# Optimization experiments

Measured on AMD Instinct MI355X. Metric: run time of the kernel, lower is better.

## Reference

```python
import jax, jax.numpy as jnp
import numpy as np

B, S, C, H, D = 2, 2048, 1024, 16, 64  # hidden C must equal H*D (value is a reshape of key_states)


def setup_inputs() -> dict:
    key = jax.random.key(0)
    ks = jax.random.split(key, 7)
    query_states = jax.random.normal(ks[0], (B, S, C), dtype=jnp.float32)
    key_states = jax.random.normal(ks[1], (B, S, C), dtype=jnp.float32)
    attention_mask = jax.random.randint(ks[2], (B, 1, 1, S), 0, 2).astype(jnp.int32)
    Wq = jax.random.normal(ks[3], (C, H, D), dtype=jnp.float32) * 0.02
    bq = jnp.zeros((H, D), dtype=jnp.float32)
    Wk = jax.random.normal(ks[4], (C, H, D), dtype=jnp.float32) * 0.02
    bk = jnp.zeros((H, D), dtype=jnp.float32)
    return {
        "query_states": query_states,
        "key_states": key_states,
        "attention_mask": attention_mask,
        "Wq": Wq,
        "bq": bq,
        "Wk": Wk,
        "bk": bk,
    }


def reference(query_states, key_states, attention_mask, Wq, bq, Wk, bk):
    # EinsumDense 'abc,cde->abde' with bias on 'de'
    q = jnp.einsum("bsc,chd->bshd", query_states, Wq) + bq  # [B,S,H,D]
    k = jnp.einsum("bsc,chd->bshd", key_states, Wk) + bk    # [B,S,H,D]
    # value is just key_states reshaped into head layout (no projection!)
    v = key_states.reshape(k.shape)                          # [B,S,H,D]
    # scale query by 1/sqrt(dk)
    q = q * jax.lax.rsqrt(jnp.asarray(D, q.dtype))
    # 'aecd,abcd->acbe': a=batch, c=head, b=query pos, e=key pos
    scores = jnp.einsum("bkhd,bqhd->bhqk", k, q)             # [B,H,Sq,Sk]
    mask = (1.0 - attention_mask.astype(scores.dtype)) * -10000.0
    scores = scores + mask
    probs = jax.nn.softmax(scores, axis=-1)
    # dropout is identity at training=False (default)
    # 'acbe,aecd->abcd': weighted sum of values over key positions
    out = jnp.einsum("bhqk,bkhd->bqhd", probs, v)            # [B,S,H,D]
    return out
```

## Files before the change

### kernel.cpp

```cpp
#include <hip/hip_runtime.h>

#define BSZ 2
#define SEQ 2048
#define CH  1024
#define NH  16
#define HD  64
#define LOG2E 1.4426950408889634f

typedef short  bf16x8 __attribute__((ext_vector_type(8)));
typedef short  bf16x4 __attribute__((ext_vector_type(4)));
typedef float  f32x4  __attribute__((ext_vector_type(4)));

__device__ __forceinline__ short f2bf(float f) {
    union { float f; unsigned u; } v; v.f = f;
    unsigned r = v.u + 0x7FFFu + ((v.u >> 16) & 1u);
    return (short)(r >> 16);
}
__device__ __forceinline__ short f2bf_fast(float f) {
    union { float f; unsigned u; } v; v.f = f;
    return (short)((v.u + 0x8000u) >> 16);
}

__global__ __launch_bounds__(256) void cast_bf16(
    const float* __restrict__ a, const float* __restrict__ b,
    short* __restrict__ da, short* __restrict__ db)
{
    const float* s = blockIdx.y ? b : a;
    short*       d = blockIdx.y ? db : da;
    long i = ((long)blockIdx.x * 256 + threadIdx.x) * 8;
    float4 v0 = *(const float4*)&s[i];
    float4 v1 = *(const float4*)&s[i + 4];
    bf16x8 o;
    o[0] = f2bf(v0.x); o[1] = f2bf(v0.y); o[2] = f2bf(v0.z); o[3] = f2bf(v0.w);
    o[4] = f2bf(v1.x); o[5] = f2bf(v1.y); o[6] = f2bf(v1.z); o[7] = f2bf(v1.w);
    *(bf16x8*)&d[i] = o;
}

__global__ __launch_bounds__(256) void transpose_cast(
    const float* __restrict__ src, short* __restrict__ dst,
    long sb0, long sb1, long db0, long db1, int srs, int drs)
{
    __shared__ float tile[64][65];
    const int z = blockIdx.z;
    const float* s = src + (long)(z >> 4) * sb0 + (long)(z & 15) * sb1;
    short*       d = dst + (long)(z >> 4) * db0 + (long)(z & 15) * db1;
    const int r0 = blockIdx.y * 64, c0 = blockIdx.x * 64;
    const int tid = threadIdx.x;
    const int r  = tid >> 2;
    const int c4 = (tid & 3) << 4;

    #pragma unroll
    for (int i = 0; i < 16; i += 4) {
        float4 v = *(const float4*)&s[(long)(r0 + r) * srs + c0 + c4 + i];
        tile[r][c4 + i + 0] = v.x;
        tile[r][c4 + i + 1] = v.y;
        tile[r][c4 + i + 2] = v.z;
        tile[r][c4 + i + 3] = v.w;
    }
    __syncthreads();
    bf16x8 o0, o1;
    #pragma unroll
    for (int i = 0; i < 8; i++) o0[i] = f2bf(tile[c4 + i][r]);
    #pragma unroll
    for (int i = 0; i < 8; i++) o1[i] = f2bf(tile[c4 + 8 + i][r]);
    *(bf16x8*)&d[(long)(c0 + r) * drs + r0 + c4 + 0] = o0;
    *(bf16x8*)&d[(long)(c0 + r) * drs + r0 + c4 + 8] = o1;
}

__global__ __launch_bounds__(256) void mask_prep(
    const int* __restrict__ am, float* __restrict__ mf)
{
    int i = blockIdx.x * 256 + threadIdx.x;
    mf[i] = (1.0f - (float)am[i]) * (-10000.0f * LOG2E);
}

__global__ __launch_bounds__(256, 2) void proj_mfma(
    const short* __restrict__ Xq, const short* __restrict__ Xk,
    const short* __restrict__ Wtq, const short* __restrict__ Wtk,
    const float* __restrict__ bq_, const float* __restrict__ bk_,
    short* __restrict__ Yq, short* __restrict__ Yk)
{
    __shared__ short At[128 * 72];
    __shared__ short Bt[128 * 72];
    const int zz = blockIdx.z;
    const short* X    = zz ? Xk  : Xq;
    const short* Wt   = zz ? Wtk : Wtq;
    const float* bias = zz ? bk_ : bq_;
    short*       Y    = zz ? Yk  : Yq;
    const float scale = zz ? 1.0f : (0.125f * LOG2E);

    const int tid  = threadIdx.x;
    const int lane = tid & 63, w = tid >> 6;
    const int quad = lane >> 4, t16 = lane & 15;
    const int m0 = blockIdx.y * 128, n0 = blockIdx.x * 128;
    const int srow = tid >> 1;
    const int shalf = (tid & 1) * 32;

    f32x4 acc[4][4];
    #pragma unroll
    for (int i = 0; i < 4; i++)
        #pragma unroll
        for (int j = 0; j < 4; j++)
            acc[i][j] = (f32x4){0.f, 0.f, 0.f, 0.f};

    const int M0 = (w >> 1) * 64, N0 = (w & 1) * 64;

    bf16x8 ar[4], br[4];
    #pragma unroll
    for (int c = 0; c < 4; c++) {
        ar[c] = *(const bf16x8*)&X [(long)(m0 + srow) * CH + shalf + 8 * c];
        br[c] = *(const bf16x8*)&Wt[(long)(n0 + srow) * CH + shalf + 8 * c];
    }

    for (int k0 = 0; k0 < CH; k0 += 64) {
        __syncthreads();
        #pragma unroll
        for (int c = 0; c < 4; c++) {
            *(bf16x8*)&At[srow * 72 + shalf + 8 * c] = ar[c];
            *(bf16x8*)&Bt[srow * 72 + shalf + 8 * c] = br[c];
        }
        __syncthreads();

        if (k0 + 64 < CH) {
            #pragma unroll
            for (int c = 0; c < 4; c++) {
                ar[c] = *(const bf16x8*)&X [(long)(m0 + srow) * CH + k0 + 64 + shalf + 8 * c];
                br[c] = *(const bf16x8*)&Wt[(long)(n0 + srow) * CH + k0 + 64 + shalf + 8 * c];
            }
        }

        #pragma unroll
        for (int kk = 0; kk < 2; kk++) {
            bf16x8 af[4], bw[4];
            #pragma unroll
            for (int im = 0; im < 4; im++)
                af[im] = *(bf16x8*)&At[(M0 + 16 * im + t16) * 72 + kk * 32 + quad * 8];
            #pragma unroll
            for (int jn = 0; jn < 4; jn++)
                bw[jn] = *(bf16x8*)&Bt[(N0 + 16 * jn + t16) * 72 + kk * 32 + quad * 8];
            #pragma unroll
            for (int im = 0; im < 4; im++)
                #pragma unroll
                for (int jn = 0; jn < 4; jn++)
                    acc[im][jn] = __builtin_amdgcn_mfma_f32_16x16x32_bf16(
                        af[im], bw[jn], acc[im][jn], 0, 0, 0);
        }
    }

    #pragma unroll
    for (int jn = 0; jn < 4; jn++) {
        float bs = bias[n0 + N0 + 16 * jn + t16];
        #pragma unroll
        for (int im = 0; im < 4; im++)
            #pragma unroll
            for (int reg = 0; reg < 4; reg++) {
                float y = (acc[im][jn][reg] + bs) * scale;
                Y[(long)(m0 + M0 + 16 * im + 4 * quad + reg) * (NH * HD)
                  + n0 + N0 + 16 * jn + t16] = f2bf(y);
            }
    }
}

__global__ __launch_bounds__(256, 4) void attn_mfma(
    const short* __restrict__ qp,
    const short* __restrict__ kp,
    const short* __restrict__ vt,
    const float* __restrict__ mf,
    float* __restrict__ out)
{
    __shared__ short Kt[64 * 72];
    __shared__ short Vt[64 * 72];
    __shared__ short Pt[64 * 72];

    const int qt0 = blockIdx.x * 64;
    const int h   = blockIdx.y;
    const int b   = blockIdx.z;
    const int tid = threadIdx.x;
    const int lane = tid & 63, w = tid >> 6;
    const int quad = lane >> 4, t16 = lane & 15;

    bf16x8 qf[2];
    #pragma unroll
    for (int ds = 0; ds < 2; ds++)
        qf[ds] = *(const bf16x8*)&qp[
            (long)(b * SEQ + qt0 + w * 16 + t16) * CH + h * HD + ds * 32 + quad * 8];

    f32x4 oa[4];
    float l_r[4];
    #pragma unroll
    for (int jt = 0; jt < 4; jt++) oa[jt] = (f32x4){0.f, 0.f, 0.f, 0.f};
    #pragma unroll
    for (int reg = 0; reg < 4; reg++) l_r[reg] = 0.f;

    const int crow = tid >> 3;
    const int ccol = (tid & 7) * 8;

    const long kbase = (long)(b * SEQ) * CH + h * HD;
    const long vbase = ((long)(b * NH + h) * HD) * SEQ;

    bf16x8 kr[2], vr[2];
    #pragma unroll
    for (int cc = 0; cc < 2; cc++) {
        int row = crow + 32 * cc;
        kr[cc] = *(const bf16x8*)&kp[kbase + (long)row * CH + ccol];
        vr[cc] = *(const bf16x8*)&vt[vbase + (long)row * SEQ + ccol];
    }

    for (int kt0 = 0; kt0 < SEQ; kt0 += 64) {
        __syncthreads();
        #pragma unroll
        for (int cc = 0; cc < 2; cc++) {
            int row = crow + 32 * cc;
            *(bf16x8*)&Kt[row * 72 + ccol] = kr[cc];
            *(bf16x8*)&Vt[row * 72 + ccol] = vr[cc];
        }
        __syncthreads();

        if (kt0 + 64 < SEQ) {
            #pragma unroll
            for (int cc = 0; cc < 2; cc++) {
                int row = crow + 32 * cc;
                kr[cc] = *(const bf16x8*)&kp[kbase + (long)(kt0 + 64 + row) * CH + ccol];
                vr[cc] = *(const bf16x8*)&vt[vbase + (long)row * SEQ + kt0 + 64 + ccol];
            }
        }

        float mv[4];
        #pragma unroll
        for (int jt = 0; jt < 4; jt++)
            mv[jt] = mf[b * SEQ + kt0 + jt * 16 + t16];

        f32x4 sa[4];
        #pragma unroll
        for (int jt = 0; jt < 4; jt++) sa[jt] = (f32x4){0.f, 0.f, 0.f, 0.f};
        #pragma unroll
        for (int ds = 0; ds < 2; ds++) {
            bf16x8 kb[4];
            #pragma unroll
            for (int jt = 0; jt < 4; jt++)
                kb[jt] = *(bf16x8*)&Kt[(jt * 16 + t16) * 72 + ds * 32 + quad * 8];
            #pragma unroll
            for (int jt = 0; jt < 4; jt++)
                sa[jt] = __builtin_amdgcn_mfma_f32_16x16x32_bf16(
                    qf[ds], kb[jt], sa[jt], 0, 0, 0);
        }

        #pragma unroll
        for (int reg = 0; reg < 4; reg++) {
            float p0 = exp2f(sa[0][reg] + mv[0]);
            float p1 = exp2f(sa[1][reg] + mv[1]);
            float p2 = exp2f(sa[2][reg] + mv[2]);
            float p3 = exp2f(sa[3][reg] + mv[3]);
            sa[0][reg] = p0; sa[1][reg] = p1;
            sa[2][reg] = p2; sa[3][reg] = p3;
            l_r[reg] += (p0 + p1) + (p2 + p3);
            int prow = (w * 16 + 4 * quad + reg) * 72;
            int sw = quad << 3;
            Pt[prow + ((0 * 16 + t16) ^ sw)] = f2bf_fast(p0);
            Pt[prow + ((1 * 16 + t16) ^ sw)] = f2bf_fast(p1);
            Pt[prow + ((2 * 16 + t16) ^ sw)] = f2bf_fast(p2);
            Pt[prow + ((3 * 16 + t16) ^ sw)] = f2bf_fast(p3);
        }

        const int rsw = ((t16 >> 2) & 3) << 3;
        #pragma unroll
        for (int ks = 0; ks < 2; ks++) {
            bf16x8 pa = *(bf16x8*)&Pt[(w * 16 + t16) * 72 + ((ks * 32 + quad * 8) ^ rsw)];
            bf16x8 vb[4];
            #pragma unroll
            for (int jt = 0; jt < 4; jt++)
                vb[jt] = *(bf16x8*)&Vt[(jt * 16 + t16) * 72 + ks * 32 + quad * 8];
            #pragma unroll
            for (int jt = 0; jt < 4; jt++)
                oa[jt] = __builtin_amdgcn_mfma_f32_16x16x32_bf16(
                    pa, vb[jt], oa[jt], 0, 0, 0);
        }
    }

    #pragma unroll
    for (int reg = 0; reg < 4; reg++) {
        float l = l_r[reg];
        #pragma unroll
        for (int off = 1; off < 16; off <<= 1)
            l += __shfl_xor(l, off, 64);
        float inv = 1.0f / l;
        int q = qt0 + w * 16 + 4 * quad + reg;
        #pragma unroll
        for (int jt = 0; jt < 4; jt++)
            out[((long)(b * SEQ + q) * NH + h) * HD + jt * 16 + t16] =
                oa[jt][reg] * inv;
    }
}

extern "C" void kernel_launch(void* const* d_in, const int* in_sizes, int n_in,
                              void* d_out, int out_size, void* d_ws, size_t ws_size,
                              hipStream_t stream) {
    const float* query = (const float*)d_in[0];
    const float* key   = (const float*)d_in[1];
    const int*   amask = (const int*)d_in[2];
    const float* Wq    = (const float*)d_in[3];
    const float* bq    = (const float*)d_in[4];
    const float* Wk    = (const float*)d_in[5];
    const float* bk    = (const float*)d_in[6];
    float* out = (float*)d_out;

    char* ws = (char*)d_ws;
    const long MB = 1024 * 1024;
    short* qc  = (short*)(ws + 0 * MB);
    short* kc  = (short*)(ws + 8 * MB);
    short* qp  = (short*)(ws + 16 * MB);
    short* kp  = (short*)(ws + 24 * MB);
    short* vtr = (short*)(ws + 32 * MB);
    short* wtq = (short*)(ws + 40 * MB);
    short* wtk = (short*)(ws + 42 * MB);
    float* mfv = (float*)(ws + 44 * MB);

    cast_bf16<<<dim3((BSZ * SEQ * CH) / 2048, 2), 256, 0, stream>>>(query, key, qc, kc);

    dim3 wt_grid(16, 16, 1);
    transpose_cast<<<wt_grid, 256, 0, stream>>>(Wq, wtq, 0, 0, 0, 0, CH, CH);
    transpose_cast<<<wt_grid, 256, 0, stream>>>(Wk, wtk, 0, 0, 0, 0, CH, CH);
    dim3 vt_grid(1, SEQ / 64, BSZ * NH);
    transpose_cast<<<vt_grid, 256, 0, stream>>>(
        key, vtr,
        (long)SEQ * CH, (long)HD,
        (long)NH * HD * SEQ, (long)HD * SEQ,
        CH, SEQ);
    mask_prep<<<dim3(BSZ * SEQ / 256), 256, 0, stream>>>(amask, mfv);

    dim3 pgrid((NH * HD) / 128, (BSZ * SEQ) / 128, 2);
    proj_mfma<<<pgrid, 256, 0, stream>>>(qc, kc, wtq, wtk, bq, bk, qp, kp);

    dim3 agrid(SEQ / 64, NH, BSZ);
    attn_mfma<<<agrid, 256, 0, stream>>>(qp, kp, vtr, mfv, out);
}
```

Before: 208.7 us.

## Compute transposed scores to keep P in registers and double query tile per block

The attention kernel now computes S^T (K as the A operand, Q as B), so each lane holds four consecutive key positions for one query. These feed straight into a 16x16x16 bf16 MFMA as the B operand of O^T = V^T P^T. This removes the shared-memory round trip for P and its barrier-free scatter writes. Each wave also handles 32 query rows instead of 16, so every K/V tile loaded to LDS is reused twice as much and the grid is halved. The costs are more registers (launch bounds lowered to 2 blocks per SIMD), smaller-K MFMAs for the PV product, and fewer blocks in the grid.

After: 206.2 us. No clear change (-1.2%).

```diff
diff --git a/kernel.cpp b/kernel.cpp
--- a/kernel.cpp
+++ b/kernel.cpp
@@ -20,6 +20,19 @@
     union { float f; unsigned u; } v; v.f = f;
     return (short)((v.u + 0x8000u) >> 16);
 }
+
+#if __has_builtin(__builtin_amdgcn_mfma_f32_16x16x16bf16_1k)
+__device__ __forceinline__ f32x4 mfma16x16x16(bf16x4 a, bf16x4 b, f32x4 c) {
+    return __builtin_amdgcn_mfma_f32_16x16x16bf16_1k(a, b, c, 0, 0, 0);
+}
+#else
+__device__ __forceinline__ f32x4 mfma16x16x16(bf16x4 a, bf16x4 b, f32x4 c) {
+    f32x4 d;
+    asm("v_mfma_f32_16x16x16_bf16 %0, %1, %2, %3"
+        : "=v"(d) : "v"(a), "v"(b), "v"(c));
+    return d;
+}
+#endif
 
 __global__ __launch_bounds__(256) void cast_bf16(
     const float* __restrict__ a, const float* __restrict__ b,
@@ -161,7 +174,7 @@
     }
 }
 
-__global__ __launch_bounds__(256, 4) void attn_mfma(
+__global__ __launch_bounds__(256, 2) void attn_mfma(
     const short* __restrict__ qp,
     const short* __restrict__ kp,
     const short* __restrict__ vt,
@@ -170,69 +183,71 @@
 {
     __shared__ short Kt[64 * 72];
     __shared__ short Vt[64 * 72];
-    __shared__ short Pt[64 * 72];
-
-    const int qt0 = blockIdx.x * 64;
+
+    const int qt0 = blockIdx.x * 128;
     const int h   = blockIdx.y;
     const int b   = blockIdx.z;
     const int tid = threadIdx.x;
     const int lane = tid & 63, w = tid >> 6;
     const int quad = lane >> 4, t16 = lane & 15;
 
-    bf16x8 qf[2];
-    #pragma unroll
-    for (int ds = 0; ds < 2; ds++)
-        qf[ds] = *(const bf16x8*)&qp[
-            (long)(b * SEQ + qt0 + w * 16 + t16) * CH + h * HD + ds * 32 + quad * 8];
-
-    f32x4 oa[4];
-    float l_r[4];
-    #pragma unroll
-    for (int jt = 0; jt < 4; jt++) oa[jt] = (f32x4){0.f, 0.f, 0.f, 0.f};
-    #pragma unroll
-    for (int reg = 0; reg < 4; reg++) l_r[reg] = 0.f;
-
-    const int crow = tid >> 3;
-    const int ccol = (tid & 7) * 8;
-
+    bf16x8 qf[2][2];
+    #pragma unroll
+    for (int qm = 0; qm < 2; qm++)
+        #pragma unroll
+        for (int ds = 0; ds < 2; ds++)
+            qf[qm][ds] = *(const bf16x8*)&qp[
+                (long)(b * SEQ + qt0 + w * 32 + qm * 16 + t16) * CH
+                + h * HD + ds * 32 + quad * 8];
+
+    f32x4 oa[4][2];
+    float l_r[2];
+    #pragma unroll
+    for (int dt = 0; dt < 4; dt++)
+        #pragma unroll
+        for (int qm = 0; qm < 2; qm++)
+            oa[dt][qm] = (f32x4){0.f, 0.f, 0.f, 0.f};
+    l_r[0] = l_r[1] = 0.f;
+
+    const int srow  = tid >> 2;
+    const int scol  = (tid & 3) * 16;
     const long kbase = (long)(b * SEQ) * CH + h * HD;
     const long vbase = ((long)(b * NH + h) * HD) * SEQ;
 
     bf16x8 kr[2], vr[2];
     #pragma unroll
-    for (int cc = 0; cc < 2; cc++) {
-        int row = crow + 32 * cc;
-        kr[cc] = *(const bf16x8*)&kp[kbase + (long)row * CH + ccol];
-        vr[cc] = *(const bf16x8*)&vt[vbase + (long)row * SEQ + ccol];
+    for (int c = 0; c < 2; c++) {
+        kr[c] = *(const bf16x8*)&kp[kbase + (long)srow * CH + scol + 8 * c];
+        vr[c] = *(const bf16x8*)&vt[vbase + (long)srow * SEQ + scol + 8 * c];
     }
 
     for (int kt0 = 0; kt0 < SEQ; kt0 += 64) {
         __syncthreads();
         #pragma unroll
-        for (int cc = 0; cc < 2; cc++) {
-            int row = crow + 32 * cc;
-            *(bf16x8*)&Kt[row * 72 + ccol] = kr[cc];
-            *(bf16x8*)&Vt[row * 72 + ccol] = vr[cc];
+        for (int c = 0; c < 2; c++) {
+            *(bf16x8*)&Kt[srow * 72 + scol + 8 * c] = kr[c];
+            *(bf16x8*)&Vt[srow * 72 + scol + 8 * c] = vr[c];
         }
         __syncthreads();
 
         if (kt0 + 64 < SEQ) {
             #pragma unroll
-            for (int cc = 0; cc < 2; cc++) {
-                int row = crow + 32 * cc;
-                kr[cc] = *(const bf16x8*)&kp[kbase + (long)(kt0 + 64 + row) * CH + ccol];
-                vr[cc] = *(const bf16x8*)&vt[vbase + (long)row * SEQ + kt0 + 64 + ccol];
+            for (int c = 0; c < 2; c++) {
+                kr[c] = *(const bf16x8*)&kp[kbase + (long)(kt0 + 64 + srow) * CH + scol + 8 * c];
+                vr[c] = *(const bf16x8*)&vt[vbase + (long)srow * SEQ + kt0 + 64 + scol + 8 * c];
             }
         }
 
-        float mv[4];
+        float4 mv4[4];
         #pragma unroll
         for (int jt = 0; jt < 4; jt++)
-            mv[jt] = mf[b * SEQ + kt0 + jt * 16 + t16];
-
-        f32x4 sa[4];
-        #pragma unroll
-        for (int jt = 0; jt < 4; jt++) sa[jt] = (f32x4){0.f, 0.f, 0.f, 0.f};
+            mv4[jt] = *(const float4*)&mf[b * SEQ + kt0 + jt * 16 + quad * 4];
+
+        f32x4 sa[2][4];
+        #pragma unroll
+        for (int qm = 0; qm < 2; qm++)
+            #pragma unroll
+            for (int jt = 0; jt < 4; jt++) sa[qm][jt] = (f32x4){0.f, 0.f, 0.f, 0.f};
         #pragma unroll
         for (int ds = 0; ds < 2; ds++) {
             bf16x8 kb[4];
@@ -240,55 +255,56 @@
             for (int jt = 0; jt < 4; jt++)
                 kb[jt] = *(bf16x8*)&Kt[(jt * 16 + t16) * 72 + ds * 32 + quad * 8];
             #pragma unroll
-            for (int jt = 0; jt < 4; jt++)
-                sa[jt] = __builtin_amdgcn_mfma_f32_16x16x32_bf16(
-                    qf[ds], kb[jt], sa[jt], 0, 0, 0);
-        }
-
-        #pragma unroll
-        for (int reg = 0; reg < 4; reg++) {
-            float p0 = exp2f(sa[0][reg] + mv[0]);
-            float p1 = exp2f(sa[1][reg] + mv[1]);
-            float p2 = exp2f(sa[2][reg] + mv[2]);
-            float p3 = exp2f(sa[3][reg] + mv[3]);
-            sa[0][reg] = p0; sa[1][reg] = p1;
-            sa[2][reg] = p2; sa[3][reg] = p3;
-            l_r[reg] += (p0 + p1) + (p2 + p3);
-            int prow = (w * 16 + 4 * quad + reg) * 72;
-            int sw = quad << 3;
-            Pt[prow + ((0 * 16 + t16) ^ sw)] = f2bf_fast(p0);
-            Pt[prow + ((1 * 16 + t16) ^ sw)] = f2bf_fast(p1);
-            Pt[prow + ((2 * 16 + t16) ^ sw)] = f2bf_fast(p2);
-            Pt[prow + ((3 * 16 + t16) ^ sw)] = f2bf_fast(p3);
-        }
-
-        const int rsw = ((t16 >> 2) & 3) << 3;
-        #pragma unroll
-        for (int ks = 0; ks < 2; ks++) {
-            bf16x8 pa = *(bf16x8*)&Pt[(w * 16 + t16) * 72 + ((ks * 32 + quad * 8) ^ rsw)];
-            bf16x8 vb[4];
-            #pragma unroll
-            for (int jt = 0; jt < 4; jt++)
-                vb[jt] = *(bf16x8*)&Vt[(jt * 16 + t16) * 72 + ks * 32 + quad * 8];
-            #pragma unroll
-            for (int jt = 0; jt < 4; jt++)
-                oa[jt] = __builtin_amdgcn_mfma_f32_16x16x32_bf16(
-                    pa, vb[jt], oa[jt], 0, 0, 0);
-        }
-    }
-
-    #pragma unroll
-    for (int reg = 0; reg < 4; reg++) {
-        float l = l_r[reg];
-        #pragma unroll
-        for (int off = 1; off < 16; off <<= 1)
-            l += __shfl_xor(l, off, 64);
+            for (int qm = 0; qm < 2; qm++)
+                #pragma unroll
+                for (int jt = 0; jt < 4; jt++)
+                    sa[qm][jt] = __builtin_amdgcn_mfma_f32_16x16x32_bf16(
+                        kb[jt], qf[qm][ds], sa[qm][jt], 0, 0, 0);
+        }
+
+        bf16x4 pb[2][4];
+        #pragma unroll
+        for (int qm = 0; qm < 2; qm++)
+            #pragma unroll
+            for (int jt = 0; jt < 4; jt++) {
+                float p0 = exp2f(sa[qm][jt][0] + mv4[jt].x);
+                float p1 = exp2f(sa[qm][jt][1] + mv4[jt].y);
+                float p2 = exp2f(sa[qm][jt][2] + mv4[jt].z);
+                float p3 = exp2f(sa[qm][jt][3] + mv4[jt].w);
+                l_r[qm] += (p0 + p1) + (p2 + p3);
+                bf16x4 pk;
+                pk[0] = f2bf_fast(p0); pk[1] = f2bf_fast(p1);
+                pk[2] = f2bf_fast(p2); pk[3] = f2bf_fast(p3);
+                pb[qm][jt] = pk;
+            }
+
+        #pragma unroll
+        for (int jt = 0; jt < 4; jt++) {
+            bf16x4 va[4];
+            #pragma unroll
+            for (int dt = 0; dt < 4; dt++)
+                va[dt] = *(bf16x4*)&Vt[(dt * 16 + t16) * 72 + jt * 16 + quad * 4];
+            #pragma unroll
+            for (int dt = 0; dt < 4; dt++)
+                #pragma unroll
+                for (int qm = 0; qm < 2; qm++)
+                    oa[dt][qm] = mfma16x16x16(va[dt], pb[qm][jt], oa[dt][qm]);
+        }
+    }
+
+    #pragma unroll
+    for (int qm = 0; qm < 2; qm++) {
+        float l = l_r[qm];
+        l += __shfl_xor(l, 16, 64);
+        l += __shfl_xor(l, 32, 64);
         float inv = 1.0f / l;
-        int q = qt0 + w * 16 + 4 * quad + reg;
-        #pragma unroll
-        for (int jt = 0; jt < 4; jt++)
-            out[((long)(b * SEQ + q) * NH + h) * HD + jt * 16 + t16] =
-                oa[jt][reg] * inv;
+        int q = qt0 + w * 32 + qm * 16 + t16;
+        #pragma unroll
+        for (int dt = 0; dt < 4; dt++) {
+            f32x4 o = oa[dt][qm];
+            float4 st = {o[0] * inv, o[1] * inv, o[2] * inv, o[3] * inv};
+            *(float4*)&out[((long)(b * SEQ + q) * NH + h) * HD + dt * 16 + quad * 4] = st;
+        }
     }
 }
 
@@ -331,6 +347,6 @@
     dim3 pgrid((NH * HD) / 128, (BSZ * SEQ) / 128, 2);
     proj_mfma<<<pgrid, 256, 0, stream>>>(qc, kc, wtq, wtk, bq, bk, qp, kp);
 
-    dim3 agrid(SEQ / 64, NH, BSZ);
+    dim3 agrid(SEQ / 128, NH, BSZ);
     attn_mfma<<<agrid, 256, 0, stream>>>(qp, kp, vtr, mfv, out);
 }
```
